# Kernel tuning notes

Hardware: AMD Instinct MI355X
Metric: run time of the kernel (lower is better)

The kernel has to match this reference:

```python
import jax, jax.numpy as jnp
import numpy as np

B, T, C, H = 128, 512, 256, 64  # batch, seq (<= BLOCK_SIZE=512), EMBED_SIZE, HEAD_SIZE


def setup_inputs() -> dict:
    key = jax.random.key(0)
    k0, k1, k2, k3 = jax.random.split(key, 4)
    # nn.Linear(C, H, bias=False) applies x @ W.T with W:[H,C]; we store the
    # transposed weight [C,H] so the math x @ W is identical.
    scale = 1.0 / np.sqrt(C)  # rough Linear-init scale, values only matter for testing
    return {
        "input_embeddings": jax.random.normal(k0, (B, T, C), dtype=jnp.float32),
        "Wq": jax.random.normal(k1, (C, H), dtype=jnp.float32) * scale,
        "Wk": jax.random.normal(k2, (C, H), dtype=jnp.float32) * scale,
        "Wv": jax.random.normal(k3, (C, H), dtype=jnp.float32) * scale,
    }


def reference(input_embeddings, Wq, Wk, Wv):
    x = input_embeddings
    t = x.shape[1]
    h = Wq.shape[1]
    q = jnp.einsum("btc,ch->bth", x, Wq)
    k = jnp.einsum("btc,ch->bth", x, Wk)
    v = jnp.einsum("btc,ch->bth", x, Wv)
    # QK^T / sqrt(H), causal mask, softmax  (faithful to masked_fill(-inf))
    sim = jnp.einsum("bth,bsh->bts", q, k) / jnp.sqrt(jnp.asarray(h, x.dtype))
    causal = jnp.tril(jnp.ones((t, t), dtype=bool))
    sim = jnp.where(causal, sim, -jnp.inf)
    wei = jax.nn.softmax(sim, axis=-1)
    out = jnp.einsum("bts,bsh->bth", wei, v)
    return out
```

## Files before the change

kernel.cpp:

```cpp
#include <hip/hip_runtime.h>
#include <hip/hip_bf16.h>
#include <math.h>

#define Bn 128
#define Tn 512
#define Cn 256
#define Hn 64
#define NQKV 192
#define XP 264
#define HP2 72
#define SCL 0.18033688011112042f

typedef __attribute__((ext_vector_type(8))) short short8v;
typedef __attribute__((ext_vector_type(4))) float float4v;

__device__ __forceinline__ ushort f2bf(float f) {
    __hip_bfloat16 h = __float2bfloat16(f);
    return *reinterpret_cast<ushort*>(&h);
}

__global__ __launch_bounds__(256) void prep_w_kernel(
    const float* __restrict__ Wq, const float* __restrict__ Wk,
    const float* __restrict__ Wv, ushort* __restrict__ wcT)
{
    const int row = blockIdx.x;
    const int c   = threadIdx.x;
    const float* W = (row < 64) ? Wq : (row < 128) ? Wk : Wv;
    const int h = row & 63;
    wcT[row * Cn + c] = f2bf(W[c * Hn + h]);
}

__global__ __launch_bounds__(256) void qkv_mfma_kernel(
    const float* __restrict__ x, const ushort* __restrict__ wcT,
    ushort* __restrict__ q, ushort* __restrict__ k, ushort* __restrict__ vT)
{
    __shared__ ushort xs[64 * XP];
    __shared__ ushort wsh[NQKV * XP];
    const int tid = threadIdx.x;
    const long row0 = (long)blockIdx.x * 64;

    {
        const uint4* w16 = (const uint4*)wcT;
        #pragma unroll
        for (int i = 0; i < 24; ++i) {
            int idx = tid + i * 256;
            int r   = idx >> 5;
            int c8  = idx & 31;
            *(uint4*)&wsh[r * XP + c8 * 8] = w16[idx];
        }
    }
    {
        const float4* x4 = (const float4*)(x + row0 * Cn);
        #pragma unroll
        for (int i = 0; i < 16; ++i) {
            int idx = tid + i * 256;
            int r   = idx >> 6;
            int c4  = idx & 63;
            float4 f = x4[idx];
            union { ushort u[4]; uint2 p; } pk;
            pk.u[0] = f2bf(f.x); pk.u[1] = f2bf(f.y);
            pk.u[2] = f2bf(f.z); pk.u[3] = f2bf(f.w);
            *(uint2*)&xs[r * XP + c4 * 4] = pk.p;
        }
    }
    __syncthreads();

    const int lane = tid & 63;
    const int wv   = tid >> 6;
    const int lr   = lane & 15;
    const int hi   = lane >> 4;

    const ushort* arow = &xs[(wv * 16 + lr) * XP + hi * 8];
    const ushort* brow = &wsh[lr * XP + hi * 8];

    float4v acc[12];
    #pragma unroll
    for (int n = 0; n < 12; ++n) acc[n] = (float4v){0.f, 0.f, 0.f, 0.f};

    #pragma unroll
    for (int ks = 0; ks < 8; ++ks) {
        short8v a = *(const short8v*)(arow + ks * 32);
        #pragma unroll
        for (int n = 0; n < 12; ++n) {
            short8v b = *(const short8v*)(brow + (n * 16) * XP + ks * 32);
            acc[n] = __builtin_amdgcn_mfma_f32_16x16x32_bf16(a, b, acc[n], 0, 0, 0);
        }
    }

    const long grow0 = row0 + wv * 16 + hi * 4;
    #pragma unroll
    for (int n = 0; n < 8; ++n) {
        int col = n * 16 + lr;
        ushort* outp = (col < 64) ? q : k;
        int hcol = col & 63;
        #pragma unroll
        for (int reg = 0; reg < 4; ++reg)
            outp[(grow0 + reg) * Hn + hcol] = f2bf(acc[n][reg]);
    }

    __syncthreads();
    ushort* Vl = xs;
    const int tloc0 = wv * 16 + hi * 4;
    #pragma unroll
    for (int n = 8; n < 12; ++n) {
        int h = (n - 8) * 16 + lr;
        #pragma unroll
        for (int reg = 0; reg < 4; ++reg)
            Vl[h * 72 + tloc0 + reg] = f2bf(acc[n][reg]);
    }
    __syncthreads();
    {
        const int bb = (int)(row0 >> 9);
        const int t0 = (int)(row0 & 511);
        #pragma unroll
        for (int i = 0; i < 2; ++i) {
            int idx = tid + i * 256;
            int h   = idx >> 3;
            int c8  = idx & 7;
            *(uint4*)(vT + ((long)bb * Hn + h) * Tn + t0 + c8 * 8) =
                *(const uint4*)&Vl[h * 72 + c8 * 8];
        }
    }
}

__global__ __launch_bounds__(512) void attn_mfma_kernel(
    const ushort* __restrict__ q, const ushort* __restrict__ k,
    const ushort* __restrict__ vT, float* __restrict__ out)
{
    __shared__ ushort Ks[64 * HP2];
    __shared__ ushort Vt[64 * HP2];
    __shared__ ushort Pl[8][16 * HP2];

    const int tid = threadIdx.x;
    const int f   = blockIdx.x;
    const int c   = f & 255;
    const int b   = c >> 1;
    const int par = c & 1;
    const int qtp = (f < 256) ? par : (3 - par);
    const int ntiles = 2 * qtp + 2;

    const long base  = (long)b * Tn * Hn;
    const int lane = tid & 63;
    const int wv   = tid >> 6;
    const int lr   = lane & 15;
    const int hi   = lane >> 4;

    const int qrow_g = qtp * 128 + wv * 16;
    const int mrow0  = qrow_g + hi * 4;

    short8v qa[2];
    {
        const ushort* qp = q + base + (long)(qrow_g + lr) * Hn + hi * 8;
        qa[0] = *(const short8v*)(qp);
        qa[1] = *(const short8v*)(qp + 32);
    }

    const int sr  = tid >> 3;
    const int sc8 = tid & 7;
    uint4 kreg = *(const uint4*)(k + base + (long)sr * Hn + sc8 * 8);
    uint4 vreg = *(const uint4*)(vT + base + (long)sr * Tn + sc8 * 8);

    float4v o[4];
    #pragma unroll
    for (int n = 0; n < 4; ++n) o[n] = (float4v){0.f, 0.f, 0.f, 0.f};
    float m[4], l[4];
    #pragma unroll
    for (int reg = 0; reg < 4; ++reg) { m[reg] = -INFINITY; l[reg] = 0.f; }

    for (int kt = 0; kt < ntiles; ++kt) {
        __syncthreads();
        *(uint4*)&Ks[sr * HP2 + sc8 * 8] = kreg;
        *(uint4*)&Vt[sr * HP2 + sc8 * 8] = vreg;
        __syncthreads();
        if (kt + 1 < ntiles) {
            kreg = *(const uint4*)(k  + base + (long)((kt + 1) * 64 + sr) * Hn + sc8 * 8);
            vreg = *(const uint4*)(vT + base + (long)sr * Tn + (kt + 1) * 64 + sc8 * 8);
        }
        if (kt * 64 > qrow_g + 15) continue;

        float4v s4[4];
        #pragma unroll
        for (int n = 0; n < 4; ++n) s4[n] = (float4v){0.f, 0.f, 0.f, 0.f};
        #pragma unroll
        for (int ks = 0; ks < 2; ++ks) {
            short8v a = qa[ks];
            #pragma unroll
            for (int n = 0; n < 4; ++n) {
                short8v bb = *(const short8v*)&Ks[(n * 16 + lr) * HP2 + ks * 32 + hi * 8];
                s4[n] = __builtin_amdgcn_mfma_f32_16x16x32_bf16(a, bb, s4[n], 0, 0, 0);
            }
        }

        const bool partial = (kt * 64 + 63 > qrow_g);
        if (partial) {
            #pragma unroll
            for (int n = 0; n < 4; ++n) {
                int kcol = kt * 64 + n * 16 + lr;
                #pragma unroll
                for (int reg = 0; reg < 4; ++reg) {
                    float y = s4[n][reg] * SCL;
                    s4[n][reg] = (kcol <= mrow0 + reg) ? y : -INFINITY;
                }
            }
        } else {
            #pragma unroll
            for (int n = 0; n < 4; ++n)
                #pragma unroll
                for (int reg = 0; reg < 4; ++reg) s4[n][reg] *= SCL;
        }

        #pragma unroll
        for (int reg = 0; reg < 4; ++reg) {
            float mx = fmaxf(fmaxf(s4[0][reg], s4[1][reg]),
                             fmaxf(s4[2][reg], s4[3][reg]));
            mx = fmaxf(mx, __shfl_xor(mx, 1));
            mx = fmaxf(mx, __shfl_xor(mx, 2));
            mx = fmaxf(mx, __shfl_xor(mx, 4));
            mx = fmaxf(mx, __shfl_xor(mx, 8));
            float mN = fmaxf(m[reg], mx);
            float sc = exp2f(m[reg] - mN);
            float ps = 0.f;
            #pragma unroll
            for (int n = 0; n < 4; ++n) {
                float p = exp2f(s4[n][reg] - mN);
                s4[n][reg] = p;
                ps += p;
            }
            ps += __shfl_xor(ps, 1);
            ps += __shfl_xor(ps, 2);
            ps += __shfl_xor(ps, 4);
            ps += __shfl_xor(ps, 8);
            l[reg] = l[reg] * sc + ps;
            m[reg] = mN;
            #pragma unroll
            for (int n = 0; n < 4; ++n) o[n][reg] *= sc;
        }

        #pragma unroll
        for (int n = 0; n < 4; ++n)
            #pragma unroll
            for (int reg = 0; reg < 4; ++reg)
                Pl[wv][(hi * 4 + reg) * HP2 + n * 16 + lr] = f2bf(s4[n][reg]);

        #pragma unroll
        for (int ks = 0; ks < 2; ++ks) {
            short8v a = *(const short8v*)&Pl[wv][lr * HP2 + ks * 32 + hi * 8];
            #pragma unroll
            for (int n = 0; n < 4; ++n) {
                short8v bb = *(const short8v*)&Vt[(n * 16 + lr) * HP2 + ks * 32 + hi * 8];
                o[n] = __builtin_amdgcn_mfma_f32_16x16x32_bf16(a, bb, o[n], 0, 0, 0);
            }
        }
    }

    #pragma unroll
    for (int reg = 0; reg < 4; ++reg) {
        float inv = 1.0f / l[reg];
        float* orow = out + base + (long)(mrow0 + reg) * Hn;
        #pragma unroll
        for (int n = 0; n < 4; ++n)
            orow[n * 16 + lr] = o[n][reg] * inv;
    }
}

extern "C" void kernel_launch(void* const* d_in, const int* in_sizes, int n_in,
                              void* d_out, int out_size, void* d_ws, size_t ws_size,
                              hipStream_t stream) {
    const float* x  = (const float*)d_in[0];
    const float* Wq = (const float*)d_in[1];
    const float* Wk = (const float*)d_in[2];
    const float* Wv = (const float*)d_in[3];
    float* out = (float*)d_out;

    const size_t n = (size_t)Bn * Tn * Hn;
    ushort* qws = (ushort*)d_ws;
    ushort* kws = qws + n;
    ushort* vTs = kws + n;

    ushort* wcT = (ushort*)d_out;

    prep_w_kernel<<<dim3(NQKV), 256, 0, stream>>>(Wq, Wk, Wv, wcT);
    qkv_mfma_kernel<<<dim3(Bn * Tn / 64), 256, 0, stream>>>(x, wcT, qws, kws, vTs);
    attn_mfma_kernel<<<dim3(512), 512, 0, stream>>>(qws, kws, vTs, out);
}
```

Measured before the change: 57.17 us.

## Restructure QKV projection: register-resident weights, persistent 256-row blocks, swizzled LDS, prefetch

```diff
diff --git a/kernel.cpp b/kernel.cpp
--- a/kernel.cpp
+++ b/kernel.cpp
@@ -7,7 +7,6 @@
 #define Cn 256
 #define Hn 64
 #define NQKV 192
-#define XP 264
 #define HP2 72
 #define SCL 0.18033688011112042f
 
@@ -30,95 +29,114 @@
     wcT[row * Cn + c] = f2bf(W[c * Hn + h]);
 }
 
-__global__ __launch_bounds__(256) void qkv_mfma_kernel(
+__global__ __launch_bounds__(512, 2) void qkv_mfma_kernel(
     const float* __restrict__ x, const ushort* __restrict__ wcT,
     ushort* __restrict__ q, ushort* __restrict__ k, ushort* __restrict__ vT)
 {
-    __shared__ ushort xs[64 * XP];
-    __shared__ ushort wsh[NQKV * XP];
-    const int tid = threadIdx.x;
-    const long row0 = (long)blockIdx.x * 64;
-
-    {
-        const uint4* w16 = (const uint4*)wcT;
-        #pragma unroll
-        for (int i = 0; i < 24; ++i) {
-            int idx = tid + i * 256;
-            int r   = idx >> 5;
-            int c8  = idx & 31;
-            *(uint4*)&wsh[r * XP + c8 * 8] = w16[idx];
-        }
-    }
-    {
-        const float4* x4 = (const float4*)(x + row0 * Cn);
-        #pragma unroll
-        for (int i = 0; i < 16; ++i) {
-            int idx = tid + i * 256;
-            int r   = idx >> 6;
-            int c4  = idx & 63;
-            float4 f = x4[idx];
-            union { ushort u[4]; uint2 p; } pk;
-            pk.u[0] = f2bf(f.x); pk.u[1] = f2bf(f.y);
-            pk.u[2] = f2bf(f.z); pk.u[3] = f2bf(f.w);
-            *(uint2*)&xs[r * XP + c4 * 4] = pk.p;
-        }
-    }
-    __syncthreads();
-
+    __shared__ ushort xlds[64 * 256];
+    __shared__ ushort Vl[64 * HP2];
+    char* xb = (char*)xlds;
+
+    const int tid  = threadIdx.x;
     const int lane = tid & 63;
     const int wv   = tid >> 6;
     const int lr   = lane & 15;
     const int hi   = lane >> 4;
-
-    const ushort* arow = &xs[(wv * 16 + lr) * XP + hi * 8];
-    const ushort* brow = &wsh[lr * XP + hi * 8];
-
-    float4v acc[12];
+    const int wr   = wv >> 2;
+    const int wc   = wv & 3;
+    const long block_row0 = (long)blockIdx.x * 256;
+
+    short8v bfr[3][8];
     #pragma unroll
-    for (int n = 0; n < 12; ++n) acc[n] = (float4v){0.f, 0.f, 0.f, 0.f};
-
-    #pragma unroll
-    for (int ks = 0; ks < 8; ++ks) {
-        short8v a = *(const short8v*)(arow + ks * 32);
-        #pragma unroll
-        for (int n = 0; n < 12; ++n) {
-            short8v b = *(const short8v*)(brow + (n * 16) * XP + ks * 32);
-            acc[n] = __builtin_amdgcn_mfma_f32_16x16x32_bf16(a, b, acc[n], 0, 0, 0);
-        }
-    }
-
-    const long grow0 = row0 + wv * 16 + hi * 4;
-    #pragma unroll
-    for (int n = 0; n < 8; ++n) {
-        int col = n * 16 + lr;
-        ushort* outp = (col < 64) ? q : k;
-        int hcol = col & 63;
-        #pragma unroll
-        for (int reg = 0; reg < 4; ++reg)
-            outp[(grow0 + reg) * Hn + hcol] = f2bf(acc[n][reg]);
-    }
-
-    __syncthreads();
-    ushort* Vl = xs;
-    const int tloc0 = wv * 16 + hi * 4;
-    #pragma unroll
-    for (int n = 8; n < 12; ++n) {
-        int h = (n - 8) * 16 + lr;
-        #pragma unroll
-        for (int reg = 0; reg < 4; ++reg)
-            Vl[h * 72 + tloc0 + reg] = f2bf(acc[n][reg]);
-    }
-    __syncthreads();
+    for (int n = 0; n < 3; ++n) {
+        const ushort* bp = wcT + (long)(wc * 48 + n * 16 + lr) * Cn + hi * 8;
+        #pragma unroll
+        for (int ks = 0; ks < 8; ++ks)
+            bfr[n][ks] = *(const short8v*)(bp + ks * 32);
+    }
+
+    float4 xr[8];
     {
-        const int bb = (int)(row0 >> 9);
-        const int t0 = (int)(row0 & 511);
-        #pragma unroll
-        for (int i = 0; i < 2; ++i) {
-            int idx = tid + i * 256;
-            int h   = idx >> 3;
-            int c8  = idx & 7;
+        const float4* x4 = (const float4*)(x + block_row0 * Cn);
+        #pragma unroll
+        for (int i = 0; i < 8; ++i) xr[i] = x4[tid + i * 512];
+    }
+
+    for (int c = 0; c < 4; ++c) {
+        #pragma unroll
+        for (int i = 0; i < 8; ++i) {
+            int idx = tid + i * 512;
+            int r   = idx >> 6;
+            int c4  = idx & 63;
+            union { ushort u[4]; uint2 p; } pk;
+            pk.u[0] = f2bf(xr[i].x); pk.u[1] = f2bf(xr[i].y);
+            pk.u[2] = f2bf(xr[i].z); pk.u[3] = f2bf(xr[i].w);
+            int off = (r * 512 + c4 * 8) ^ ((r & 7) << 4);
+            *(uint2*)(xb + off) = pk.p;
+        }
+        __syncthreads();
+
+        float4 xn[8];
+        if (c < 3) {
+            const float4* x4 = (const float4*)(x + (block_row0 + (c + 1) * 64) * Cn);
+            #pragma unroll
+            for (int i = 0; i < 8; ++i) xn[i] = x4[tid + i * 512];
+        }
+
+        float4v acc[2][3];
+        #pragma unroll
+        for (int s = 0; s < 2; ++s)
+            #pragma unroll
+            for (int n = 0; n < 3; ++n) acc[s][n] = (float4v){0.f,0.f,0.f,0.f};
+
+        #pragma unroll
+        for (int ks = 0; ks < 8; ++ks) {
+            int r0 = wr * 32 + lr;
+            int r1 = r0 + 16;
+            short8v a0 = *(const short8v*)(xb + ((r0 * 512 + ks * 64 + hi * 16) ^ ((r0 & 7) << 4)));
+            short8v a1 = *(const short8v*)(xb + ((r1 * 512 + ks * 64 + hi * 16) ^ ((r1 & 7) << 4)));
+            #pragma unroll
+            for (int n = 0; n < 3; ++n) {
+                acc[0][n] = __builtin_amdgcn_mfma_f32_16x16x32_bf16(a0, bfr[n][ks], acc[0][n], 0, 0, 0);
+                acc[1][n] = __builtin_amdgcn_mfma_f32_16x16x32_bf16(a1, bfr[n][ks], acc[1][n], 0, 0, 0);
+            }
+        }
+
+        const long rows0 = block_row0 + c * 64;
+        #pragma unroll
+        for (int s = 0; s < 2; ++s) {
+            #pragma unroll
+            for (int n = 0; n < 3; ++n) {
+                int col = wc * 48 + n * 16 + lr;
+                int tl  = wr * 32 + s * 16 + hi * 4;
+                if (col < 128) {
+                    ushort* outp = (col < 64) ? q : k;
+                    int hcol = col & 63;
+                    #pragma unroll
+                    for (int reg = 0; reg < 4; ++reg)
+                        outp[(rows0 + tl + reg) * Hn + hcol] = f2bf(acc[s][n][reg]);
+                } else {
+                    int h = col - 128;
+                    #pragma unroll
+                    for (int reg = 0; reg < 4; ++reg)
+                        Vl[h * HP2 + tl + reg] = f2bf(acc[s][n][reg]);
+                }
+            }
+        }
+        __syncthreads();
+
+        {
+            const int bb = (int)(rows0 >> 9);
+            const int t0 = (int)(rows0 & 511);
+            int h  = tid >> 3;
+            int c8 = tid & 7;
             *(uint4*)(vT + ((long)bb * Hn + h) * Tn + t0 + c8 * 8) =
-                *(const uint4*)&Vl[h * 72 + c8 * 8];
+                *(const uint4*)&Vl[h * HP2 + c8 * 8];
+        }
+
+        if (c < 3) {
+            #pragma unroll
+            for (int i = 0; i < 8; ++i) xr[i] = xn[i];
         }
     }
 }
@@ -280,6 +298,6 @@
     ushort* wcT = (ushort*)d_out;
 
     prep_w_kernel<<<dim3(NQKV), 256, 0, stream>>>(Wq, Wk, Wv, wcT);
-    qkv_mfma_kernel<<<dim3(Bn * Tn / 64), 256, 0, stream>>>(x, wcT, qws, kws, vTs);
+    qkv_mfma_kernel<<<dim3(256), 512, 0, stream>>>(x, wcT, qws, kws, vTs);
     attn_mfma_kernel<<<dim3(512), 512, 0, stream>>>(qws, kws, vTs, out);
 }
```

New measurement: 54.15 us. -5.3%, faster.
